# Kernel tuning notes

Hardware: AMD Instinct MI355X
Metric: run time of the kernel (lower is better)

The kernel has to match this reference:

```python
import jax, jax.numpy as jnp
import numpy as np

B, S1, S2, D1, D2, F = 8, 2048, 2048, 512, 512, 256

def setup_inputs() -> dict:
    key = jax.random.key(0)
    ks = jax.random.split(key, 10)
    sc1 = 1.0 / np.sqrt(D1)
    sc2 = 1.0 / np.sqrt(D2)
    scf = 1.0 / np.sqrt(F)
    return {
        "feat1": jax.random.normal(ks[0], (B, S1, D1), jnp.float32),
        "feat2": jax.random.normal(ks[1], (B, S2, D2), jnp.float32),
        "Wq": jax.random.normal(ks[2], (D1, F), jnp.float32) * sc1,
        "bq": jnp.zeros((F,), jnp.float32),
        "Wk": jax.random.normal(ks[3], (D2, F), jnp.float32) * sc2,
        "bk": jnp.zeros((F,), jnp.float32),
        "Wv": jax.random.normal(ks[4], (D2, F), jnp.float32) * sc2,
        "bv": jnp.zeros((F,), jnp.float32),
        "Wfc": jax.random.normal(ks[5], (F, F), jnp.float32) * scf,
        "bfc": jnp.zeros((F,), jnp.float32),
    }

def reference(feat1, feat2, Wq, bq, Wk, bk, Wv, bv, Wfc, bfc):
    Q = jnp.einsum('bsd,df->bsf', feat1, Wq) + bq          # [B,S1,F]
    K = jnp.einsum('btd,df->btf', feat2, Wk) + bk          # [B,S2,F]
    V = jnp.einsum('btd,df->btf', feat2, Wv) + bv          # [B,S2,F]
    scores = jnp.einsum('bsf,btf->bst', Q, K) / jnp.sqrt(jnp.float32(K.shape[-1]))
    attn = jax.nn.softmax(scores, axis=-1)                 # [B,S1,S2]
    attn_out = jnp.einsum('bst,btf->bsf', attn, V)         # [B,S1,F]
    out = jnp.einsum('bsf,fg->bsg', attn_out, Wfc) + bfc   # [B,S1,F]
    return out
```

## Files before the change

kernel.cpp:

```cpp
#include <hip/hip_runtime.h>
#include <hip/hip_bf16.h>

#define B_ 8
#define S1_ 2048
#define S2_ 2048
#define D_ 512
#define F_ 256

typedef __attribute__((ext_vector_type(4))) float f32x4;
typedef __attribute__((ext_vector_type(8))) short s16x8;
typedef __attribute__((ext_vector_type(4))) short s16x4;
typedef __attribute__((ext_vector_type(2))) int i32x2;

__device__ __forceinline__ short f2bf(float x) {
  union { float f; unsigned u; } v; v.f = x;
  unsigned r = v.u + 0x7fffu + ((v.u >> 16) & 1u);
  return (short)(r >> 16);
}

__device__ __forceinline__ int pk2bf(float a, float b) {
  union { __hip_bfloat162 h; int i; } u;
  u.h = __float22bfloat162_rn(make_float2(a, b));
  return u.i;
}

__global__ __launch_bounds__(256) void wtrans_kernel(
    const float* __restrict__ Wq, const float* __restrict__ Wk,
    const float* __restrict__ Wv, const float* __restrict__ Wfc,
    short* __restrict__ Wqt, short* __restrict__ Wkt,
    short* __restrict__ Wvt, short* __restrict__ Wfct) {
  int y = blockIdx.y;
  const float* W; short* Wt; int dl;
  if (y == 0)      { W = Wq;  Wt = Wqt;  dl = 9; }
  else if (y == 1) { W = Wk;  Wt = Wkt;  dl = 9; }
  else if (y == 2) { W = Wv;  Wt = Wvt;  dl = 9; }
  else             { W = Wfc; Wt = Wfct; dl = 8; }
  int idx = blockIdx.x * 256 + threadIdx.x;
  if (idx >= (F_ << dl)) return;
  int d = idx & ((1 << dl) - 1);
  int f = idx >> dl;
  Wt[idx] = f2bf(W[(size_t)d * F_ + f]);
}

__global__ __launch_bounds__(256, 3) void proj_kernel(
    const float* __restrict__ feat1, const float* __restrict__ feat2,
    const short* __restrict__ Wqt, const short* __restrict__ Wkt,
    const short* __restrict__ Wvt,
    const float* __restrict__ bq, const float* __restrict__ bk,
    const float* __restrict__ bv,
    short* __restrict__ Qw, short* __restrict__ Kw, short* __restrict__ Vtw) {
  const float* A; const short* Wt; const float* bias; short* outp;
  float scale; int trans;
  if (blockIdx.y == 0)      { A = feat1; Wt = Wqt; bias = bq; outp = Qw;  scale = 0.0625f; trans = 0; }
  else if (blockIdx.y == 1) { A = feat2; Wt = Wkt; bias = bk; outp = Kw;  scale = 1.0f;    trans = 0; }
  else                      { A = feat2; Wt = Wvt; bias = bv; outp = Vtw; scale = 1.0f;    trans = 1; }

  __shared__ __align__(16) short As[64][72];
  __shared__ __align__(16) short Ws[256][72];

  int m0 = blockIdx.x * 64;
  int t = threadIdx.x;
  int w = t >> 6, L = t & 63, rowA = L & 15, quad = L >> 4;
  int ar = t >> 2, ac16 = (t & 3) * 16;

  f32x4 acc[4][4];
  for (int i = 0; i < 4; ++i)
    for (int j = 0; j < 4; ++j) acc[i][j] = (f32x4){0.f, 0.f, 0.f, 0.f};

  for (int k0 = 0; k0 < D_; k0 += 64) {
    {
      const float* src = A + (size_t)(m0 + ar) * D_ + k0 + ac16;
      f32x4 v0 = *(const f32x4*)(src);
      f32x4 v1 = *(const f32x4*)(src + 4);
      f32x4 v2 = *(const f32x4*)(src + 8);
      f32x4 v3 = *(const f32x4*)(src + 12);
      s16x8 s0, s1;
      ((int*)&s0)[0] = pk2bf(v0[0], v0[1]); ((int*)&s0)[1] = pk2bf(v0[2], v0[3]);
      ((int*)&s0)[2] = pk2bf(v1[0], v1[1]); ((int*)&s0)[3] = pk2bf(v1[2], v1[3]);
      ((int*)&s1)[0] = pk2bf(v2[0], v2[1]); ((int*)&s1)[1] = pk2bf(v2[2], v2[3]);
      ((int*)&s1)[2] = pk2bf(v3[0], v3[1]); ((int*)&s1)[3] = pk2bf(v3[2], v3[3]);
      *(s16x8*)(&As[ar][ac16]) = s0;
      *(s16x8*)(&As[ar][ac16 + 8]) = s1;
    }
    for (int p = 0; p < 4; ++p) {
      int r = (t >> 2) + p * 64;
      const short* src = Wt + (size_t)r * D_ + k0 + ac16;
      *(s16x8*)(&Ws[r][ac16]) = *(const s16x8*)(src);
      *(s16x8*)(&Ws[r][ac16 + 8]) = *(const s16x8*)(src + 8);
    }
    __syncthreads();
    for (int kt = 0; kt < 2; ++kt) {
      s16x8 a[4];
      for (int mt = 0; mt < 4; ++mt)
        a[mt] = *(const s16x8*)(&As[mt * 16 + rowA][kt * 32 + quad * 8]);
      for (int nt = 0; nt < 4; ++nt) {
        s16x8 bfr = *(const s16x8*)(&Ws[w * 64 + nt * 16 + rowA][kt * 32 + quad * 8]);
        for (int mt = 0; mt < 4; ++mt)
          acc[mt][nt] = __builtin_amdgcn_mfma_f32_16x16x32_bf16(a[mt], bfr, acc[mt][nt], 0, 0, 0);
      }
    }
    __syncthreads();
  }

  if (!trans) {
    float bn[4];
    for (int nt = 0; nt < 4; ++nt) bn[nt] = bias[w * 64 + nt * 16 + rowA];
    for (int mt = 0; mt < 4; ++mt) {
      int m = m0 + mt * 16 + quad * 4;
      for (int nt = 0; nt < 4; ++nt) {
        int n = w * 64 + nt * 16 + rowA;
        for (int r = 0; r < 4; ++r)
          outp[(size_t)(m + r) * F_ + n] = f2bf((acc[mt][nt][r] + bn[nt]) * scale);
      }
    }
  } else {
    int bb = m0 >> 11;
    int tbase = m0 & (S2_ - 1);
    float bn[4];
    for (int nt = 0; nt < 4; ++nt) bn[nt] = bias[w * 64 + nt * 16 + rowA];
    for (int nt = 0; nt < 4; ++nt) {
      int f = w * 64 + nt * 16 + rowA;
      for (int mt = 0; mt < 4; ++mt) {
        int tt = tbase + mt * 16 + quad * 4;
        s16x4 o;
        for (int r = 0; r < 4; ++r) o[r] = f2bf(acc[mt][nt][r] + bn[nt]);
        *(s16x4*)(outp + ((size_t)bb * F_ + f) * S2_ + tt) = o;
      }
    }
  }
}

__global__ __launch_bounds__(512, 2) void flash_kernel(
    const short* __restrict__ Q,
    const short* __restrict__ K,
    const short* __restrict__ Vt,
    short* __restrict__ O) {
  __shared__ __align__(16) short Ks[2][64][264];
  __shared__ __align__(16) short Vs[2][256][72];
  __shared__ __align__(16) short Ps[2][64][72];

  int b = blockIdx.x >> 5;
  int s0 = (blockIdx.x & 31) * 64;
  int t = threadIdx.x;
  int w = t >> 6, L = t & 63, rowA = L & 15, quad = L >> 4;
  int isS = (w < 4);

  const short* Kb = K + (size_t)b * S2_ * F_;
  const short* Vb = Vt + (size_t)b * F_ * S2_;

  int kr = t >> 5, kc8 = (t & 31) * 8;
  int vr = t >> 3, vc8 = (t & 7) * 8;

  int rs = (w & 1) * 32, cs = ((w >> 1) & 1) * 32;
  int mg = (w - 4) & 1, fg = ((w - 4) >> 1) & 1;

  s16x8 qf[2][8];
  if (isS) {
    const short* Qb = Q + ((size_t)b * S1_ + s0 + rs) * F_;
    for (int mt = 0; mt < 2; ++mt)
      for (int kt = 0; kt < 8; ++kt)
        qf[mt][kt] = *(const s16x8*)(Qb + (size_t)(mt * 16 + rowA) * F_ + kt * 32 + quad * 8);
  }
  f32x4 o[2][8];
  for (int i = 0; i < 2; ++i)
    for (int j = 0; j < 8; ++j) o[i][j] = (f32x4){0.f, 0.f, 0.f, 0.f};
  float l_lane[2][4] = {{0.f,0.f,0.f,0.f},{0.f,0.f,0.f,0.f}};

  s16x8 kpre[4], vpre[4];
  for (int p = 0; p < 4; ++p)
    kpre[p] = *(const s16x8*)(Kb + (size_t)(kr + p * 16) * F_ + kc8);
  for (int p = 0; p < 4; ++p)
    *(s16x8*)(&Ks[0][kr + p * 16][kc8]) = kpre[p];
  for (int p = 0; p < 4; ++p)
    kpre[p] = *(const s16x8*)(Kb + (size_t)(64 + kr + p * 16) * F_ + kc8);
  for (int p = 0; p < 4; ++p)
    vpre[p] = *(const s16x8*)(Vb + (size_t)(vr + p * 64) * S2_ + vc8);

  for (int it = 0; it <= 32; ++it) {
    int cb = it & 1;
    __syncthreads();
    if (it < 32) {
      for (int p = 0; p < 4; ++p)
        *(s16x8*)(&Vs[cb][vr + p * 64][vc8]) = vpre[p];
      if (it < 31) {
        for (int p = 0; p < 4; ++p)
          *(s16x8*)(&Ks[1 - cb][kr + p * 16][kc8]) = kpre[p];
        int n0 = (it + 1) * 64;
        for (int p = 0; p < 4; ++p)
          vpre[p] = *(const s16x8*)(Vb + (size_t)(vr + p * 64) * S2_ + n0 + vc8);
      }
      if (it < 30) {
        int n0 = (it + 2) * 64;
        for (int p = 0; p < 4; ++p)
          kpre[p] = *(const s16x8*)(Kb + (size_t)(n0 + kr + p * 16) * F_ + kc8);
      }
    }
    if (isS) {
      if (it < 32) {
        f32x4 s[2][2];
        for (int i = 0; i < 2; ++i)
          for (int j = 0; j < 2; ++j) s[i][j] = (f32x4){0.f, 0.f, 0.f, 0.f};
        for (int kt = 0; kt < 8; ++kt) {
          s16x8 bf0 = *(const s16x8*)(&Ks[cb][cs + rowA][kt * 32 + quad * 8]);
          s16x8 bf1 = *(const s16x8*)(&Ks[cb][cs + 16 + rowA][kt * 32 + quad * 8]);
          for (int mt = 0; mt < 2; ++mt) {
            s[mt][0] = __builtin_amdgcn_mfma_f32_16x16x32_bf16(qf[mt][kt], bf0, s[mt][0], 0, 0, 0);
            s[mt][1] = __builtin_amdgcn_mfma_f32_16x16x32_bf16(qf[mt][kt], bf1, s[mt][1], 0, 0, 0);
          }
        }
        for (int mt = 0; mt < 2; ++mt)
          for (int nt = 0; nt < 2; ++nt)
            for (int r = 0; r < 4; ++r) {
              float p = __expf(s[mt][nt][r]);
              l_lane[mt][r] += p;
              Ps[cb][rs + mt * 16 + quad * 4 + r][cs + nt * 16 + rowA] = f2bf(p);
            }
      }
    } else {
      if (it > 0) {
        int pb = 1 - cb;
        s16x8 pa[2][2];
        for (int mt = 0; mt < 2; ++mt)
          for (int kt = 0; kt < 2; ++kt)
            pa[mt][kt] = *(const s16x8*)(&Ps[pb][mg * 32 + mt * 16 + rowA][kt * 32 + quad * 8]);
        for (int ft = 0; ft < 8; ++ft)
          for (int kt = 0; kt < 2; ++kt) {
            s16x8 vf = *(const s16x8*)(&Vs[pb][fg * 128 + ft * 16 + rowA][kt * 32 + quad * 8]);
            for (int mt = 0; mt < 2; ++mt)
              o[mt][ft] = __builtin_amdgcn_mfma_f32_16x16x32_bf16(pa[mt][kt], vf, o[mt][ft], 0, 0, 0);
          }
      }
    }
  }

  float* lf = (float*)&Ks[0][0][0];
  if (isS) {
    for (int mt = 0; mt < 2; ++mt)
      for (int r = 0; r < 4; ++r) {
        float x = l_lane[mt][r];
        for (int off = 1; off < 16; off <<= 1)
          x += __shfl_xor(x, off, 64);
        if (rowA == 0)
          lf[((w >> 1) & 1) * 64 + rs + mt * 16 + quad * 4 + r] = x;
      }
  }
  __syncthreads();
  if (!isS) {
    short* Ob = O + ((size_t)b * S1_ + s0) * F_;
    for (int mt = 0; mt < 2; ++mt)
      for (int r = 0; r < 4; ++r) {
        int row = mg * 32 + mt * 16 + quad * 4 + r;
        float inv = 1.0f / (lf[row] + lf[64 + row]);
        for (int ft = 0; ft < 8; ++ft)
          Ob[(size_t)row * F_ + fg * 128 + ft * 16 + rowA] = f2bf(o[mt][ft][r] * inv);
      }
  }
}

__global__ __launch_bounds__(256) void fc_kernel(
    const short* __restrict__ AO,
    const short* __restrict__ Wt,
    const float* __restrict__ bias,
    float* __restrict__ out) {
  __shared__ __align__(16) short As[128][72];
  __shared__ __align__(16) short Ws[128][72];

  int m0 = blockIdx.x * 128;
  int n0 = blockIdx.y * 128;
  int t = threadIdx.x;
  int w = t >> 6, L = t & 63, rowA = L & 15, quad = L >> 4;
  int wy = w >> 1, wx = w & 1;
  int srow = t >> 3, sc8 = (t & 7) * 8;

  f32x4 acc[4][4];
  for (int i = 0; i < 4; ++i)
    for (int j = 0; j < 4; ++j) acc[i][j] = (f32x4){0.f, 0.f, 0.f, 0.f};

  for (int k0 = 0; k0 < F_; k0 += 64) {
    for (int p = 0; p < 4; ++p) {
      int r = p * 32 + srow;
      *(s16x8*)(&As[r][sc8]) = *(const s16x8*)(AO + (size_t)(m0 + r) * F_ + k0 + sc8);
      *(s16x8*)(&Ws[r][sc8]) = *(const s16x8*)(Wt + (size_t)(n0 + r) * F_ + k0 + sc8);
    }
    __syncthreads();
    for (int kt = 0; kt < 2; ++kt) {
      s16x8 a[4];
      for (int mt = 0; mt < 4; ++mt)
        a[mt] = *(const s16x8*)(&As[wy * 64 + mt * 16 + rowA][kt * 32 + quad * 8]);
      for (int nt = 0; nt < 4; ++nt) {
        s16x8 bfr = *(const s16x8*)(&Ws[wx * 64 + nt * 16 + rowA][kt * 32 + quad * 8]);
        for (int mt = 0; mt < 4; ++mt)
          acc[mt][nt] = __builtin_amdgcn_mfma_f32_16x16x32_bf16(a[mt], bfr, acc[mt][nt], 0, 0, 0);
      }
    }
    __syncthreads();
  }

  float bn[4];
  for (int nt = 0; nt < 4; ++nt) bn[nt] = bias[n0 + wx * 64 + nt * 16 + rowA];
  for (int mt = 0; mt < 4; ++mt) {
    int m = m0 + wy * 64 + mt * 16 + quad * 4;
    for (int nt = 0; nt < 4; ++nt) {
      int n = n0 + wx * 64 + nt * 16 + rowA;
      for (int r = 0; r < 4; ++r)
        out[(size_t)(m + r) * F_ + n] = acc[mt][nt][r] + bn[nt];
    }
  }
}

extern "C" void kernel_launch(void* const* d_in, const int* in_sizes, int n_in,
                              void* d_out, int out_size, void* d_ws, size_t ws_size,
                              hipStream_t stream) {
  const float* feat1 = (const float*)d_in[0];
  const float* feat2 = (const float*)d_in[1];
  const float* Wq  = (const float*)d_in[2];
  const float* bq  = (const float*)d_in[3];
  const float* Wk  = (const float*)d_in[4];
  const float* bk  = (const float*)d_in[5];
  const float* Wv  = (const float*)d_in[6];
  const float* bv  = (const float*)d_in[7];
  const float* Wfc = (const float*)d_in[8];
  const float* bfc = (const float*)d_in[9];
  float* out = (float*)d_out;
  char* ws = (char*)d_ws;

  short* Qw   = (short*)(ws);
  short* Kw   = (short*)(ws + (size_t)(8u  << 20));
  short* Vtw  = (short*)(ws + (size_t)(16u << 20));
  short* AOw  = (short*)(ws + (size_t)(24u << 20));
  short* Wqt  = (short*)(ws + (size_t)(32u << 20));
  short* Wkt  = Wqt + 256 * 512;
  short* Wvt  = Wkt + 256 * 512;
  short* Wfct = Wvt + 256 * 512;

  wtrans_kernel<<<dim3(512, 4), 256, 0, stream>>>(Wq, Wk, Wv, Wfc, Wqt, Wkt, Wvt, Wfct);
  proj_kernel<<<dim3(256, 3), 256, 0, stream>>>(feat1, feat2, Wqt, Wkt, Wvt,
                                                bq, bk, bv, Qw, Kw, Vtw);
  flash_kernel<<<dim3(256), 512, 0, stream>>>(Qw, Kw, Vtw, AOw);
  fc_kernel<<<dim3(128, 2), 256, 0, stream>>>(AOw, Wfct, bfc, out);
}
```

Baseline: 195.5 us.

## Fuse FC into flash epilogue, tile weight transpose, prefetch in projection

The output FC GEMM is folded into the flash-attention epilogue. The normalized attention tile is staged in shared memory as bf16 and multiplied by Wfc there, so the AO round trip to global memory and a separate kernel launch go away. The weight-transpose kernel now uses 64x64 shared-memory tiles for coalesced reads and writes. The projection kernel moves to 512 threads with register prefetch of the next K slice. In exchange, the flash kernel gains a longer serial tail and reuses its LDS buffers for the FC stage.

```diff
diff --git a/kernel.cpp b/kernel.cpp
--- a/kernel.cpp
+++ b/kernel.cpp
@@ -10,7 +10,6 @@
 typedef __attribute__((ext_vector_type(4))) float f32x4;
 typedef __attribute__((ext_vector_type(8))) short s16x8;
 typedef __attribute__((ext_vector_type(4))) short s16x4;
-typedef __attribute__((ext_vector_type(2))) int i32x2;
 
 __device__ __forceinline__ short f2bf(float x) {
   union { float f; unsigned u; } v; v.f = x;
@@ -30,19 +29,46 @@
     short* __restrict__ Wqt, short* __restrict__ Wkt,
     short* __restrict__ Wvt, short* __restrict__ Wfct) {
   int y = blockIdx.y;
-  const float* W; short* Wt; int dl;
-  if (y == 0)      { W = Wq;  Wt = Wqt;  dl = 9; }
-  else if (y == 1) { W = Wk;  Wt = Wkt;  dl = 9; }
-  else if (y == 2) { W = Wv;  Wt = Wvt;  dl = 9; }
-  else             { W = Wfc; Wt = Wfct; dl = 8; }
-  int idx = blockIdx.x * 256 + threadIdx.x;
-  if (idx >= (F_ << dl)) return;
-  int d = idx & ((1 << dl) - 1);
-  int f = idx >> dl;
-  Wt[idx] = f2bf(W[(size_t)d * F_ + f]);
-}
-
-__global__ __launch_bounds__(256, 3) void proj_kernel(
+  const float* W; short* Wt; int D;
+  if (y == 0)      { W = Wq;  Wt = Wqt;  D = 512; }
+  else if (y == 1) { W = Wk;  Wt = Wkt;  D = 512; }
+  else if (y == 2) { W = Wv;  Wt = Wvt;  D = 512; }
+  else             { W = Wfc; Wt = Wfct; D = 256; }
+  int tiles_d = D >> 6;
+  int bx = blockIdx.x;
+  if (bx >= tiles_d * 4) return;
+  int d0 = (bx % tiles_d) * 64, f0 = (bx / tiles_d) * 64;
+
+  __shared__ short Ts[64][68];
+  int t = threadIdx.x;
+  int r = t >> 2, c16 = (t & 3) * 16;
+  {
+    const float* src = W + (size_t)(d0 + r) * F_ + f0 + c16;
+    f32x4 v0 = *(const f32x4*)(src);
+    f32x4 v1 = *(const f32x4*)(src + 4);
+    f32x4 v2 = *(const f32x4*)(src + 8);
+    f32x4 v3 = *(const f32x4*)(src + 12);
+    s16x8 s0, s1;
+    ((int*)&s0)[0] = pk2bf(v0[0], v0[1]); ((int*)&s0)[1] = pk2bf(v0[2], v0[3]);
+    ((int*)&s0)[2] = pk2bf(v1[0], v1[1]); ((int*)&s0)[3] = pk2bf(v1[2], v1[3]);
+    ((int*)&s1)[0] = pk2bf(v2[0], v2[1]); ((int*)&s1)[1] = pk2bf(v2[2], v2[3]);
+    ((int*)&s1)[2] = pk2bf(v3[0], v3[1]); ((int*)&s1)[3] = pk2bf(v3[2], v3[3]);
+    *(s16x8*)(&Ts[r][c16]) = s0;
+    *(s16x8*)(&Ts[r][c16 + 8]) = s1;
+  }
+  __syncthreads();
+  {
+    int fr = t >> 2, dc16 = (t & 3) * 16;
+    s16x8 o0, o1;
+    for (int j = 0; j < 8; ++j) o0[j] = Ts[dc16 + j][fr];
+    for (int j = 0; j < 8; ++j) o1[j] = Ts[dc16 + 8 + j][fr];
+    short* dst = Wt + (size_t)(f0 + fr) * D + d0 + dc16;
+    *(s16x8*)dst = o0;
+    *(s16x8*)(dst + 8) = o1;
+  }
+}
+
+__global__ __launch_bounds__(512, 2) void proj_kernel(
     const float* __restrict__ feat1, const float* __restrict__ feat2,
     const short* __restrict__ Wqt, const short* __restrict__ Wkt,
     const short* __restrict__ Wvt,
@@ -56,46 +82,53 @@
   else                      { A = feat2; Wt = Wvt; bias = bv; outp = Vtw; scale = 1.0f;    trans = 1; }
 
   __shared__ __align__(16) short As[64][72];
-  __shared__ __align__(16) short Ws[256][72];
+  __shared__ __align__(16) short Ws2[256][72];
 
   int m0 = blockIdx.x * 64;
   int t = threadIdx.x;
   int w = t >> 6, L = t & 63, rowA = L & 15, quad = L >> 4;
-  int ar = t >> 2, ac16 = (t & 3) * 16;
-
-  f32x4 acc[4][4];
-  for (int i = 0; i < 4; ++i)
+  int wy = w & 1, wx = w >> 1;
+
+  int ar = t >> 3, ac8 = (t & 7) * 8;
+  int wr = t >> 1, wc32 = (t & 1) * 32;
+
+  f32x4 av0, av1;
+  s16x8 wv[4];
+  {
+    const float* asrc = A + (size_t)(m0 + ar) * D_ + ac8;
+    av0 = *(const f32x4*)(asrc);
+    av1 = *(const f32x4*)(asrc + 4);
+    const short* wsrc = Wt + (size_t)wr * D_ + wc32;
+    for (int j = 0; j < 4; ++j) wv[j] = *(const s16x8*)(wsrc + j * 8);
+  }
+
+  f32x4 acc[2][4];
+  for (int i = 0; i < 2; ++i)
     for (int j = 0; j < 4; ++j) acc[i][j] = (f32x4){0.f, 0.f, 0.f, 0.f};
 
   for (int k0 = 0; k0 < D_; k0 += 64) {
     {
-      const float* src = A + (size_t)(m0 + ar) * D_ + k0 + ac16;
-      f32x4 v0 = *(const f32x4*)(src);
-      f32x4 v1 = *(const f32x4*)(src + 4);
-      f32x4 v2 = *(const f32x4*)(src + 8);
-      f32x4 v3 = *(const f32x4*)(src + 12);
-      s16x8 s0, s1;
-      ((int*)&s0)[0] = pk2bf(v0[0], v0[1]); ((int*)&s0)[1] = pk2bf(v0[2], v0[3]);
-      ((int*)&s0)[2] = pk2bf(v1[0], v1[1]); ((int*)&s0)[3] = pk2bf(v1[2], v1[3]);
-      ((int*)&s1)[0] = pk2bf(v2[0], v2[1]); ((int*)&s1)[1] = pk2bf(v2[2], v2[3]);
-      ((int*)&s1)[2] = pk2bf(v3[0], v3[1]); ((int*)&s1)[3] = pk2bf(v3[2], v3[3]);
-      *(s16x8*)(&As[ar][ac16]) = s0;
-      *(s16x8*)(&As[ar][ac16 + 8]) = s1;
-    }
-    for (int p = 0; p < 4; ++p) {
-      int r = (t >> 2) + p * 64;
-      const short* src = Wt + (size_t)r * D_ + k0 + ac16;
-      *(s16x8*)(&Ws[r][ac16]) = *(const s16x8*)(src);
-      *(s16x8*)(&Ws[r][ac16 + 8]) = *(const s16x8*)(src + 8);
-    }
-    __syncthreads();
+      s16x8 s;
+      ((int*)&s)[0] = pk2bf(av0[0], av0[1]); ((int*)&s)[1] = pk2bf(av0[2], av0[3]);
+      ((int*)&s)[2] = pk2bf(av1[0], av1[1]); ((int*)&s)[3] = pk2bf(av1[2], av1[3]);
+      *(s16x8*)(&As[ar][ac8]) = s;
+      for (int j = 0; j < 4; ++j) *(s16x8*)(&Ws2[wr][wc32 + j * 8]) = wv[j];
+    }
+    __syncthreads();
+    if (k0 + 64 < D_) {
+      const float* asrc = A + (size_t)(m0 + ar) * D_ + k0 + 64 + ac8;
+      av0 = *(const f32x4*)(asrc);
+      av1 = *(const f32x4*)(asrc + 4);
+      const short* wsrc = Wt + (size_t)wr * D_ + k0 + 64 + wc32;
+      for (int j = 0; j < 4; ++j) wv[j] = *(const s16x8*)(wsrc + j * 8);
+    }
     for (int kt = 0; kt < 2; ++kt) {
-      s16x8 a[4];
-      for (int mt = 0; mt < 4; ++mt)
-        a[mt] = *(const s16x8*)(&As[mt * 16 + rowA][kt * 32 + quad * 8]);
+      s16x8 a[2];
+      for (int mt = 0; mt < 2; ++mt)
+        a[mt] = *(const s16x8*)(&As[wy * 32 + mt * 16 + rowA][kt * 32 + quad * 8]);
       for (int nt = 0; nt < 4; ++nt) {
-        s16x8 bfr = *(const s16x8*)(&Ws[w * 64 + nt * 16 + rowA][kt * 32 + quad * 8]);
-        for (int mt = 0; mt < 4; ++mt)
+        s16x8 bfr = *(const s16x8*)(&Ws2[wx * 64 + nt * 16 + rowA][kt * 32 + quad * 8]);
+        for (int mt = 0; mt < 2; ++mt)
           acc[mt][nt] = __builtin_amdgcn_mfma_f32_16x16x32_bf16(a[mt], bfr, acc[mt][nt], 0, 0, 0);
       }
     }
@@ -104,11 +137,11 @@
 
   if (!trans) {
     float bn[4];
-    for (int nt = 0; nt < 4; ++nt) bn[nt] = bias[w * 64 + nt * 16 + rowA];
-    for (int mt = 0; mt < 4; ++mt) {
-      int m = m0 + mt * 16 + quad * 4;
+    for (int nt = 0; nt < 4; ++nt) bn[nt] = bias[wx * 64 + nt * 16 + rowA];
+    for (int mt = 0; mt < 2; ++mt) {
+      int m = m0 + wy * 32 + mt * 16 + quad * 4;
       for (int nt = 0; nt < 4; ++nt) {
-        int n = w * 64 + nt * 16 + rowA;
+        int n = wx * 64 + nt * 16 + rowA;
         for (int r = 0; r < 4; ++r)
           outp[(size_t)(m + r) * F_ + n] = f2bf((acc[mt][nt][r] + bn[nt]) * scale);
       }
@@ -117,11 +150,11 @@
     int bb = m0 >> 11;
     int tbase = m0 & (S2_ - 1);
     float bn[4];
-    for (int nt = 0; nt < 4; ++nt) bn[nt] = bias[w * 64 + nt * 16 + rowA];
+    for (int nt = 0; nt < 4; ++nt) bn[nt] = bias[wx * 64 + nt * 16 + rowA];
     for (int nt = 0; nt < 4; ++nt) {
-      int f = w * 64 + nt * 16 + rowA;
-      for (int mt = 0; mt < 4; ++mt) {
-        int tt = tbase + mt * 16 + quad * 4;
+      int f = wx * 64 + nt * 16 + rowA;
+      for (int mt = 0; mt < 2; ++mt) {
+        int tt = tbase + wy * 32 + mt * 16 + quad * 4;
         s16x4 o;
         for (int r = 0; r < 4; ++r) o[r] = f2bf(acc[mt][nt][r] + bn[nt]);
         *(s16x4*)(outp + ((size_t)bb * F_ + f) * S2_ + tt) = o;
@@ -134,7 +167,9 @@
     const short* __restrict__ Q,
     const short* __restrict__ K,
     const short* __restrict__ Vt,
-    short* __restrict__ O) {
+    const short* __restrict__ Wfct,
+    const float* __restrict__ bfc,
+    float* __restrict__ out) {
   __shared__ __align__(16) short Ks[2][64][264];
   __shared__ __align__(16) short Vs[2][256][72];
   __shared__ __align__(16) short Ps[2][64][72];
@@ -233,7 +268,10 @@
     }
   }
 
-  float* lf = (float*)&Ks[0][0][0];
+  float* lf = (float*)&Ps[0][0][0];
+  short (*Os)[264] = (short(*)[264])&Ks[0][0][0];
+  short (*Wg)[72] = (short(*)[72])&Vs[0][0][0];
+
   if (isS) {
     for (int mt = 0; mt < 2; ++mt)
       for (int r = 0; r < 4; ++r) {
@@ -246,65 +284,52 @@
   }
   __syncthreads();
   if (!isS) {
-    short* Ob = O + ((size_t)b * S1_ + s0) * F_;
     for (int mt = 0; mt < 2; ++mt)
       for (int r = 0; r < 4; ++r) {
         int row = mg * 32 + mt * 16 + quad * 4 + r;
         float inv = 1.0f / (lf[row] + lf[64 + row]);
         for (int ft = 0; ft < 8; ++ft)
-          Ob[(size_t)row * F_ + fg * 128 + ft * 16 + rowA] = f2bf(o[mt][ft][r] * inv);
-      }
-  }
-}
-
-__global__ __launch_bounds__(256) void fc_kernel(
-    const short* __restrict__ AO,
-    const short* __restrict__ Wt,
-    const float* __restrict__ bias,
-    float* __restrict__ out) {
-  __shared__ __align__(16) short As[128][72];
-  __shared__ __align__(16) short Ws[128][72];
-
-  int m0 = blockIdx.x * 128;
-  int n0 = blockIdx.y * 128;
-  int t = threadIdx.x;
-  int w = t >> 6, L = t & 63, rowA = L & 15, quad = L >> 4;
-  int wy = w >> 1, wx = w & 1;
-  int srow = t >> 3, sc8 = (t & 7) * 8;
-
-  f32x4 acc[4][4];
-  for (int i = 0; i < 4; ++i)
-    for (int j = 0; j < 4; ++j) acc[i][j] = (f32x4){0.f, 0.f, 0.f, 0.f};
-
-  for (int k0 = 0; k0 < F_; k0 += 64) {
-    for (int p = 0; p < 4; ++p) {
-      int r = p * 32 + srow;
-      *(s16x8*)(&As[r][sc8]) = *(const s16x8*)(AO + (size_t)(m0 + r) * F_ + k0 + sc8);
-      *(s16x8*)(&Ws[r][sc8]) = *(const s16x8*)(Wt + (size_t)(n0 + r) * F_ + k0 + sc8);
-    }
-    __syncthreads();
-    for (int kt = 0; kt < 2; ++kt) {
-      s16x8 a[4];
-      for (int mt = 0; mt < 4; ++mt)
-        a[mt] = *(const s16x8*)(&As[wy * 64 + mt * 16 + rowA][kt * 32 + quad * 8]);
-      for (int nt = 0; nt < 4; ++nt) {
-        s16x8 bfr = *(const s16x8*)(&Ws[wx * 64 + nt * 16 + rowA][kt * 32 + quad * 8]);
-        for (int mt = 0; mt < 4; ++mt)
-          acc[mt][nt] = __builtin_amdgcn_mfma_f32_16x16x32_bf16(a[mt], bfr, acc[mt][nt], 0, 0, 0);
-      }
-    }
-    __syncthreads();
-  }
-
-  float bn[4];
-  for (int nt = 0; nt < 4; ++nt) bn[nt] = bias[n0 + wx * 64 + nt * 16 + rowA];
-  for (int mt = 0; mt < 4; ++mt) {
-    int m = m0 + wy * 64 + mt * 16 + quad * 4;
-    for (int nt = 0; nt < 4; ++nt) {
-      int n = n0 + wx * 64 + nt * 16 + rowA;
-      for (int r = 0; r < 4; ++r)
-        out[(size_t)(m + r) * F_ + n] = acc[mt][nt][r] + bn[nt];
-    }
+          Os[row][fg * 128 + ft * 16 + rowA] = f2bf(o[mt][ft][r] * inv);
+      }
+  }
+  __syncthreads();
+
+  int fr = w & 3, gh = w >> 2;
+  s16x8 af[8];
+  for (int kt = 0; kt < 8; ++kt)
+    af[kt] = *(const s16x8*)(&Os[fr * 16 + rowA][kt * 32 + quad * 8]);
+  f32x4 acc[8];
+  for (int i = 0; i < 8; ++i) acc[i] = (f32x4){0.f, 0.f, 0.f, 0.f};
+
+  int sr = t >> 1, sc32 = (t & 1) * 32;
+  for (int kc = 0; kc < 4; ++kc) {
+    const short* wsrc = Wfct + (size_t)sr * F_ + kc * 64 + sc32;
+    s16x8 w0 = *(const s16x8*)(wsrc);
+    s16x8 w1 = *(const s16x8*)(wsrc + 8);
+    s16x8 w2 = *(const s16x8*)(wsrc + 16);
+    s16x8 w3 = *(const s16x8*)(wsrc + 24);
+    *(s16x8*)(&Wg[sr][sc32])      = w0;
+    *(s16x8*)(&Wg[sr][sc32 + 8])  = w1;
+    *(s16x8*)(&Wg[sr][sc32 + 16]) = w2;
+    *(s16x8*)(&Wg[sr][sc32 + 24]) = w3;
+    __syncthreads();
+    for (int nt = 0; nt < 8; ++nt) {
+      int g = gh * 128 + nt * 16 + rowA;
+      s16x8 b0 = *(const s16x8*)(&Wg[g][quad * 8]);
+      s16x8 b1 = *(const s16x8*)(&Wg[g][32 + quad * 8]);
+      acc[nt] = __builtin_amdgcn_mfma_f32_16x16x32_bf16(af[kc * 2], b0, acc[nt], 0, 0, 0);
+      acc[nt] = __builtin_amdgcn_mfma_f32_16x16x32_bf16(af[kc * 2 + 1], b1, acc[nt], 0, 0, 0);
+    }
+    __syncthreads();
+  }
+
+  float bn[8];
+  for (int nt = 0; nt < 8; ++nt) bn[nt] = bfc[gh * 128 + nt * 16 + rowA];
+  float* Ob = out + ((size_t)b * S1_ + s0 + fr * 16) * F_;
+  for (int nt = 0; nt < 8; ++nt) {
+    int g = gh * 128 + nt * 16 + rowA;
+    for (int r = 0; r < 4; ++r)
+      Ob[(size_t)(quad * 4 + r) * F_ + g] = acc[nt][r] + bn[nt];
   }
 }
 
@@ -327,15 +352,13 @@
   short* Qw   = (short*)(ws);
   short* Kw   = (short*)(ws + (size_t)(8u  << 20));
   short* Vtw  = (short*)(ws + (size_t)(16u << 20));
-  short* AOw  = (short*)(ws + (size_t)(24u << 20));
   short* Wqt  = (short*)(ws + (size_t)(32u << 20));
   short* Wkt  = Wqt + 256 * 512;
   short* Wvt  = Wkt + 256 * 512;
   short* Wfct = Wvt + 256 * 512;
 
-  wtrans_kernel<<<dim3(512, 4), 256, 0, stream>>>(Wq, Wk, Wv, Wfc, Wqt, Wkt, Wvt, Wfct);
-  proj_kernel<<<dim3(256, 3), 256, 0, stream>>>(feat1, feat2, Wqt, Wkt, Wvt,
+  wtrans_kernel<<<dim3(32, 4), 256, 0, stream>>>(Wq, Wk, Wv, Wfc, Wqt, Wkt, Wvt, Wfct);
+  proj_kernel<<<dim3(256, 3), 512, 0, stream>>>(feat1, feat2, Wqt, Wkt, Wvt,
                                                 bq, bk, bv, Qw, Kw, Vtw);
-  flash_kernel<<<dim3(256), 512, 0, stream>>>(Qw, Kw, Vtw, AOw);
-  fc_kernel<<<dim3(128, 2), 256, 0, stream>>>(AOw, Wfct, bfc, out);
-}
+  flash_kernel<<<dim3(256), 512, 0, stream>>>(Qw, Kw, Vtw, Wfct, bfc, out);
+}
```

Result: no change. 199.3 us (+1.9%).
